# Performance work log

Hardware: AMD Instinct MI355X
Metric: run time of the kernel (lower is better)

The kernel has to match this reference:

```python
import jax, jax.numpy as jnp
import numpy as np

B, S, FEAT = 64, 196, 512
D_MODEL, D_INPUT = 1024, 512
HEADS = 8          # cross-attention heads
SYNC_HEADS = 8     # neuron-sync attention heads (num_attn_heads)
ITERS = 50         # thought ticks
MEM = 25           # memory_length
NLM_H = 16         # memory_hidden_dims
OUT = 1000         # out_dims


def _n(key, i, shape, scale=0.02):
    return scale * jax.random.normal(jax.random.fold_in(key, i), shape, dtype=jnp.float32)


def setup_inputs() -> dict:
    key = jax.random.key(0)
    return {
        "x": jax.random.normal(jax.random.fold_in(key, 0), (B, S, FEAT), dtype=jnp.float32),
        "kv_w": _n(key, 1, (D_INPUT, FEAT)), "kv_b": jnp.zeros((D_INPUT,), jnp.float32),
        "ln_kv_s": jnp.ones((D_INPUT,), jnp.float32), "ln_kv_b": jnp.zeros((D_INPUT,), jnp.float32),
        "q_w": _n(key, 2, (D_INPUT, D_MODEL)), "q_b": jnp.zeros((D_INPUT,), jnp.float32),
        "in_proj_w": _n(key, 3, (3 * D_INPUT, D_INPUT)), "in_proj_b": jnp.zeros((3 * D_INPUT,), jnp.float32),
        "out_proj_w": _n(key, 4, (D_INPUT, D_INPUT)), "out_proj_b": jnp.zeros((D_INPUT,), jnp.float32),
        "W_q": _n(key, 5, (D_MODEL, D_MODEL), 0.03), "W_k": _n(key, 6, (D_MODEL, D_MODEL), 0.03),
        "W_v": _n(key, 7, (D_MODEL, D_MODEL), 0.03),
        "syn_w": _n(key, 8, (2 * D_MODEL, D_INPUT + D_MODEL)), "syn_b": jnp.zeros((2 * D_MODEL,), jnp.float32),
        "syn_ln_s": jnp.ones((D_MODEL,), jnp.float32), "syn_ln_b": jnp.zeros((D_MODEL,), jnp.float32),
        "nlm_w1": _n(key, 9, (MEM, 2 * NLM_H, D_MODEL), 0.1), "nlm_b1": jnp.zeros((D_MODEL, 2 * NLM_H), jnp.float32),
        "nlm_w2": _n(key, 10, (NLM_H, 2, D_MODEL), 0.1), "nlm_b2": jnp.zeros((D_MODEL, 2), jnp.float32),
        "start_activated_state": _n(key, 11, (D_MODEL,), 0.03),
        "start_trace": _n(key, 12, (D_MODEL, MEM), 0.03),
        "out_w": _n(key, 13, (OUT, D_MODEL)), "out_b": jnp.zeros((OUT,), jnp.float32),
    }


def _ln(x, s, b, eps=1e-5):
    m = x.mean(-1, keepdims=True)
    v = x.var(-1, keepdims=True)
    return (x - m) / jnp.sqrt(v + eps) * s + b


def _glu(x):
    a, g = jnp.split(x, 2, axis=-1)
    return a * jax.nn.sigmoid(g)


def reference(x, kv_w, kv_b, ln_kv_s, ln_kv_b, q_w, q_b, in_proj_w, in_proj_b,
              out_proj_w, out_proj_b, W_q, W_k, W_v, syn_w, syn_b, syn_ln_s, syn_ln_b,
              nlm_w1, nlm_b1, nlm_w2, nlm_b2, start_activated_state, start_trace,
              out_w, out_b):
    b = x.shape[0]
    dh_sync = D_MODEL // SYNC_HEADS
    dh = D_INPUT // HEADS

    # kv_proj: Linear + LayerNorm over backbone features (backbone='none')
    kv = _ln(x @ kv_w.T + kv_b, ln_kv_s, ln_kv_b)  # (B,S,Di)
    wq_c, wk_c, wv_c = jnp.split(in_proj_w, 3, axis=0)
    bq_c, bk_c, bv_c = jnp.split(in_proj_b, 3, axis=0)
    Kc = (kv @ wk_c.T + bk_c).reshape(b, S, HEADS, dh).transpose(0, 2, 1, 3)  # (B,H,S,dh)
    Vc = (kv @ wv_c.T + bv_c).reshape(b, S, HEADS, dh).transpose(0, 2, 1, 3)

    def sync_attn(hist, cur):
        # hist: (B,D,T) post-activation history; cur: (B,D) current post-activations
        hr = jnp.swapaxes(hist, 1, 2)  # (B,T,D)
        T = hr.shape[1]
        Q = (hr @ W_q.T).reshape(b, T, SYNC_HEADS, dh_sync).transpose(0, 2, 1, 3)  # (B,H,T,dh)
        K = (hr @ W_k.T).reshape(b, T, SYNC_HEADS, dh_sync).transpose(0, 2, 1, 3)
        V = (cur @ W_v.T).reshape(b, SYNC_HEADS, dh_sync)  # (B,H,dh)
        # neuron-vs-neuron scores: (B,H,dh,dh)
        scores = jnp.einsum('bhtd,bhte->bhde', Q, K) / jnp.sqrt(jnp.float32(dh_sync))
        w = jax.nn.softmax(scores, axis=-1)
        att = jnp.einsum('bhde,bhe->bhd', w, V)  # (B,H,dh)
        # torch: attended.transpose(1,2).reshape(B, D)
        return att.transpose(0, 2, 1).reshape(b, D_MODEL)

    def cross_attn(sync_a):
        q = sync_a @ q_w.T + q_b  # (B,Di)
        Qh = (q @ wq_c.T + bq_c).reshape(b, HEADS, 1, dh)
        s = jnp.einsum('bhqd,bhkd->bhqk', Qh, Kc) / jnp.sqrt(jnp.float32(dh))
        w = jax.nn.softmax(s, axis=-1)
        o = jnp.einsum('bhqk,bhkd->bhqd', w, Vc).transpose(0, 2, 1, 3).reshape(b, D_INPUT)
        return o @ out_proj_w.T + out_proj_b

    state_trace0 = jnp.broadcast_to(start_trace[None], (b, D_MODEL, MEM))
    act0 = jnp.broadcast_to(start_activated_state[None], (b, D_MODEL))
    hist0 = jnp.broadcast_to(start_activated_state[None, :, None], (b, D_MODEL, MEM))
    log_nc = jnp.log(jnp.float32(OUT))

    def tick(carry, _):
        st, act, hist = carry
        sync_a = sync_attn(hist, act)                     # action synchronisation
        ao = cross_attn(sync_a)                           # (B,Di)
        pre = jnp.concatenate([ao, act], axis=-1)
        state = _ln(_glu(pre @ syn_w.T + syn_b), syn_ln_s, syn_ln_b)  # synapse MLP (depth 1)
        st = jnp.concatenate([st[:, :, 1:], state[:, :, None]], axis=-1)  # sliding pre-act trace
        # per-neuron deep NLM (SuperLinear einsums)
        h = _glu(jnp.einsum('bdm,mhd->bdh', st, nlm_w1) + nlm_b1)
        act_new = _glu(jnp.einsum('bdh,hod->bdo', h, nlm_w2) + nlm_b2)[..., 0]
        hist = jnp.concatenate([hist[:, :, 1:], act_new[:, :, None]], axis=-1)
        sync_o = sync_attn(hist, act_new)                 # output synchronisation
        pred = sync_o @ out_w.T + out_b
        logp = jax.nn.log_softmax(pred, axis=-1)
        ne = -jnp.sum(jnp.exp(logp) * logp, axis=-1) / log_nc
        cert = jnp.stack([ne, 1.0 - ne], axis=-1)
        return (st, act_new, hist), (pred, cert, sync_o)

    _, (preds, certs, syncs) = jax.lax.scan(tick, (state_trace0, act0, hist0), None, length=ITERS)
    predictions = jnp.transpose(preds, (1, 2, 0))  # (B,OUT,T)
    certainties = jnp.transpose(certs, (1, 2, 0))  # (B,2,T)
    return predictions, certainties, syncs[-1]
```

## Files before the change

kernel.cpp:

```cpp
#include <hip/hip_runtime.h>
#include <hip/hip_bf16.h>

typedef __attribute__((ext_vector_type(8))) short short8v;
typedef __attribute__((ext_vector_type(4))) float f32x4;
typedef __attribute__((ext_vector_type(4))) float float4v;

#define DEV __device__ __forceinline__

DEV short f2bfs(float x){
  union { float f; unsigned u; } v; v.f = x;
  unsigned r = (v.u + 0x7FFFu + ((v.u >> 16) & 1u)) >> 16;
  return (short)(unsigned short)r;
}
DEV float bfs2f(short s){
  union { unsigned u; float f; } v; v.u = ((unsigned)(unsigned short)s) << 16;
  return v.f;
}
DEV float sigm(float x){ return 1.f / (1.f + __expf(-x)); }
DEV int zmap(int j){ int g = (j >= 1024) ? 1 : 0; int i = j - (g << 10); return (i & 15) + ((i >> 4) << 5) + (g << 4); }

DEV int aldi(const void* p){ return __hip_atomic_load((const int*)p, __ATOMIC_RELAXED, __HIP_MEMORY_SCOPE_AGENT); }
DEV float aldf(const void* p){ return __hip_atomic_load((const float*)p, __ATOMIC_RELAXED, __HIP_MEMORY_SCOPE_AGENT); }
DEV long long aldll(const void* p){ return __hip_atomic_load((const long long*)p, __ATOMIC_RELAXED, __HIP_MEMORY_SCOPE_AGENT); }

DEV void gbar(unsigned* bar, int nb){
  __syncthreads();
  if (threadIdx.x == 0){
    __builtin_amdgcn_fence(__ATOMIC_RELEASE, "agent");
    unsigned* gen = bar + 128;
    unsigned g = __hip_atomic_load(gen, __ATOMIC_RELAXED, __HIP_MEMORY_SCOPE_AGENT);
    int lane = blockIdx.x & 7;
    __hip_atomic_fetch_add(bar + lane*16, 1u, __ATOMIC_RELAXED, __HIP_MEMORY_SCOPE_AGENT);
    if (blockIdx.x == 0){
      unsigned sum;
      do {
        sum = 0;
#pragma unroll
        for (int i = 0; i < 8; i++) sum += __hip_atomic_load(bar + i*16, __ATOMIC_RELAXED, __HIP_MEMORY_SCOPE_AGENT);
      } while (sum < (unsigned)nb);
#pragma unroll
      for (int i = 0; i < 8; i++) __hip_atomic_store(bar + i*16, 0u, __ATOMIC_RELAXED, __HIP_MEMORY_SCOPE_AGENT);
      __hip_atomic_store(gen, g + 1u, __ATOMIC_RELEASE, __HIP_MEMORY_SCOPE_AGENT);
    } else {
      while (__hip_atomic_load(gen, __ATOMIC_RELAXED, __HIP_MEMORY_SCOPE_AGENT) == g)
        __builtin_amdgcn_s_sleep(1);
    }
  }
  __syncthreads();
}


DEV void phase_qhcross(int u, const short* __restrict__ Wfq, const float* __restrict__ bfq,
    const short* __restrict__ Kc, const short* __restrict__ Vc, const short* __restrict__ S_bf,
    short* __restrict__ oaC, float* __restrict__ stats, float* smf, int tid, int zero_stats)
{
  float* Srow = smf;
  float* qs   = smf + 1024;
  float* wsm  = smf + 1088;
  float* red  = smf + 1344;
  int h = u & 7, b = u >> 3;
  __syncthreads();
  const int* spi = (const int*)(S_bf + b*1024);
#pragma unroll
  for (int r = 0; r < 2; r++){
    int idx = tid + r*256;
    int pv = aldi(spi + idx);
    Srow[idx*2]     = bfs2f((short)(pv & 0xffff));
    Srow[idx*2 + 1] = bfs2f((short)(((unsigned)pv) >> 16));
  }
  if (zero_stats && tid < 128) stats[tid] = 0.f;
  __syncthreads();
  {
    int d = tid & 63, c = tid >> 6;
    const short* wp = Wfq + (size_t)(h*64 + d)*1024 + c*256;
    const float* srp = Srow + c*256;
    float acc = 0.f;
#pragma unroll 4
    for (int i = 0; i < 256; i += 8){
      short8v wv = *(const short8v*)(wp + i);
#pragma unroll
      for (int j = 0; j < 8; j++) acc += bfs2f(wv[j]) * srp[i + j];
    }
    red[tid] = acc;
  }
  __syncthreads();
  if (tid < 64) qs[tid] = bfq[h*64 + tid] + red[tid] + red[tid+64] + red[tid+128] + red[tid+192];
  __syncthreads();
  float sv = -1e30f;
  if (tid < 196){
    const short* kp = Kc + ((size_t)(b*196 + tid)*512 + h*64);
    float acc = 0.f;
#pragma unroll
    for (int j = 0; j < 64; j += 8){
      short8v kv8 = *(const short8v*)(kp + j);
#pragma unroll
      for (int u8 = 0; u8 < 8; u8++) acc += bfs2f(kv8[u8]) * qs[j + u8];
    }
    sv = acc * 0.125f;
  }
  red[tid] = sv; __syncthreads();
  for (int s = 128; s > 0; s >>= 1){ if (tid < s) red[tid] = fmaxf(red[tid], red[tid+s]); __syncthreads(); }
  float M = red[0]; __syncthreads();
  float e = (tid < 196) ? __expf(sv - M) : 0.f;
  wsm[tid] = e; red[tid] = e; __syncthreads();
  for (int s = 128; s > 0; s >>= 1){ if (tid < s) red[tid] += red[tid+s]; __syncthreads(); }
  float Z = red[0]; __syncthreads();
  int dd = tid & 63, cc = tid >> 6;
  float acc = 0.f;
  for (int s = cc; s < 196; s += 4) acc += wsm[s] * bfs2f(Vc[(size_t)(b*196 + s)*512 + h*64 + dd]);
  red[tid] = acc; __syncthreads();
  if (tid < 64){
    float o = (red[tid] + red[tid+64] + red[tid+128] + red[tid+192]) / Z;
    oaC[(size_t)b*1536 + h*64 + tid] = f2bfs(o);
  }
  __syncthreads();
}

DEV void phase_glu(int u, const short* __restrict__ Wz, const float* __restrict__ bz,
    const short* __restrict__ oaC, float* __restrict__ ubuf, float* __restrict__ stats,
    float* smf, int tid)
{
  float* part   = smf;
  float* statsl = smf + 8192;
  int n0 = u * 32;
  __syncthreads();
  if (tid < 128) statsl[tid] = 0.f;
  int w = tid >> 6, l15 = tid & 15, l4 = (tid >> 4) & 3;
  f32x4 acc[4][2];
#pragma unroll
  for (int mi = 0; mi < 4; mi++)
#pragma unroll
    for (int ni = 0; ni < 2; ni++) acc[mi][ni] = (f32x4){0.f,0.f,0.f,0.f};
#pragma unroll 2
  for (int it = 0; it < 12; it++){
    int ks = w*384 + it*32 + l4*8;
    short8v a4[4], bb[2];
#pragma unroll
    for (int mi = 0; mi < 4; mi++)
      a4[mi] = *(const short8v*)(oaC + (size_t)(mi*16 + l15)*1536 + ks);
#pragma unroll
    for (int ni = 0; ni < 2; ni++)
      bb[ni] = *(const short8v*)(Wz + (size_t)(n0 + ni*16 + l15)*1536 + ks);
#pragma unroll
    for (int mi = 0; mi < 4; mi++)
#pragma unroll
      for (int ni = 0; ni < 2; ni++)
        acc[mi][ni] = __builtin_amdgcn_mfma_f32_16x16x32_bf16(a4[mi], bb[ni], acc[mi][ni], 0, 0, 0);
  }
#pragma unroll
  for (int mi = 0; mi < 4; mi++)
#pragma unroll
    for (int ni = 0; ni < 2; ni++)
#pragma unroll
      for (int r = 0; r < 4; r++)
        part[w*2048 + (mi*16 + l4*4 + r)*32 + ni*16 + l15] = acc[mi][ni][r];
  __syncthreads();
  int m = tid >> 2;
  float s1 = 0.f, s2 = 0.f;
#pragma unroll
  for (int e = 0; e < 4; e++){
    int j = ((tid & 3) << 2) + e;
    float a = part[m*32 + j] + part[2048 + m*32 + j] + part[4096 + m*32 + j] + part[6144 + m*32 + j] + bz[n0 + j];
    float g = part[m*32 + 16 + j] + part[2048 + m*32 + 16 + j] + part[4096 + m*32 + 16 + j] + part[6144 + m*32 + 16 + j] + bz[n0 + 16 + j];
    float uv = a * sigm(g);
    ubuf[(size_t)m*1024 + (n0 >> 1) + j] = uv;
    s1 += uv; s2 += uv*uv;
  }
  atomicAdd(&statsl[m], s1); atomicAdd(&statsl[64 + m], s2);
  __syncthreads();
  if (tid < 64){ atomicAdd(&stats[tid], statsl[tid]); atomicAdd(&stats[64 + tid], statsl[64 + tid]); }
  __syncthreads();
}

DEV void phase_nlm(int u, const float* __restrict__ ubuf, const float* __restrict__ stats,
    const float* __restrict__ g_s, const float* __restrict__ g_b, float* __restrict__ st,
    const float* __restrict__ w1, const float* __restrict__ b1,
    const float* __restrict__ w2, const float* __restrict__ b2,
    short* __restrict__ oaN, int t, float* smf, int tid)
{
  float* pl = smf;
  int x = u & 63, y = u >> 6;
  int d_i = tid & 15, b_i = (tid >> 4) & 7, half = tid >> 7;
  int d = x*16 + d_i, b = y*8 + b_i;
  float mu = aldf(stats + b) * (1.f/1024.f);
  float var = aldf(stats + 64 + b) * (1.f/1024.f) - mu*mu;
  float rs = rsqrtf(var + 1e-5f);
  float uv = aldf(ubuf + b*1024 + d);
  float state = (uv - mu)*rs*g_s[d] + g_b[d];
  int slot = t % 25;
  if (half == 0) st[(size_t)slot*65536 + b*1024 + d] = state;
  float pre[16];
#pragma unroll
  for (int hh = 0; hh < 16; hh++) pre[hh] = b1[d*32 + half*16 + hh];
  int p0 = (t + 1) % 25;
#pragma unroll 5
  for (int m = 0; m < 25; m++){
    int p = p0 + m; if (p >= 25) p -= 25;
    float sm = (p == slot) ? state : st[(size_t)p*65536 + b*1024 + d];
#pragma unroll
    for (int hh = 0; hh < 16; hh++) pre[hh] += sm * w1[(size_t)(m*32 + half*16 + hh)*1024 + d];
  }
  __syncthreads();
#pragma unroll
  for (int hh = 0; hh < 16; hh++) pl[((half*8 + b_i)*16 + hh)*16 + d_i] = pre[hh];
  __syncthreads();
  if (half == 0){
    float p2a = b2[d*2 + 0], p2g = b2[d*2 + 1];
#pragma unroll
    for (int i = 0; i < 16; i++){
      float hv = pl[((b_i)*16 + i)*16 + d_i] * sigm(pl[((8 + b_i)*16 + i)*16 + d_i]);
      p2a += hv * w2[(size_t)(i*2 + 0)*1024 + d];
      p2g += hv * w2[(size_t)(i*2 + 1)*1024 + d];
    }
    float act = p2a * sigm(p2g);
    oaN[(size_t)b*1536 + 512 + d] = f2bfs(act);
  }
  __syncthreads();
}

DEV void phase_qkv(int u, const short* __restrict__ Wqkv, const short* __restrict__ act_bf,
    short* __restrict__ Qb, short* __restrict__ Kb, float* __restrict__ vc, int slot,
    float* smf, int tid)
{
  float* part = smf;
  int n0 = u * 32;
  __syncthreads();
  int w = tid >> 6, l15 = tid & 15, l4 = (tid >> 4) & 3;
  f32x4 acc[4][2];
#pragma unroll
  for (int mi = 0; mi < 4; mi++)
#pragma unroll
    for (int ni = 0; ni < 2; ni++) acc[mi][ni] = (f32x4){0.f,0.f,0.f,0.f};
#pragma unroll 2
  for (int it = 0; it < 8; it++){
    int ks = w*256 + it*32 + l4*8;
    short8v a4[4], bb[2];
#pragma unroll
    for (int mi = 0; mi < 4; mi++)
      a4[mi] = *(const short8v*)(act_bf + (size_t)(mi*16 + l15)*1536 + ks);
#pragma unroll
    for (int ni = 0; ni < 2; ni++)
      bb[ni] = *(const short8v*)(Wqkv + (size_t)(n0 + ni*16 + l15)*1024 + ks);
#pragma unroll
    for (int mi = 0; mi < 4; mi++)
#pragma unroll
      for (int ni = 0; ni < 2; ni++)
        acc[mi][ni] = __builtin_amdgcn_mfma_f32_16x16x32_bf16(a4[mi], bb[ni], acc[mi][ni], 0, 0, 0);
  }
#pragma unroll
  for (int mi = 0; mi < 4; mi++)
#pragma unroll
    for (int ni = 0; ni < 2; ni++)
#pragma unroll
      for (int r = 0; r < 4; r++)
        part[w*2048 + (mi*16 + l4*4 + r)*32 + ni*16 + l15] = acc[mi][ni][r];
  __syncthreads();
  int m = tid >> 2;
#pragma unroll
  for (int e = 0; e < 8; e++){
    int nl = ((tid & 3) << 3) + e;
    float v = part[m*32 + nl] + part[2048 + m*32 + nl] + part[4096 + m*32 + nl] + part[6144 + m*32 + nl];
    int n = n0 + nl;
    if (n < 1024)      Qb[((size_t)m*1024 + n)*32 + slot] = f2bfs(v);
    else if (n < 2048) Kb[((size_t)m*1024 + (n-1024))*32 + slot] = f2bfs(v);
    else               vc[(size_t)m*1024 + (n-2048)] = v;
  }
  __syncthreads();
}

DEV void phase_sync(int u, int t, const short* __restrict__ Qbuf, const short* __restrict__ Kbuf,
    const float* __restrict__ vcur, float* __restrict__ S, short* __restrict__ S_bf,
    short* __restrict__ SyncO, float* smf, int tid)
{
  short8v* qlds = (short8v*)smf;
  short8v* klds = ((short8v*)smf) + 512;
  long long* ql = (long long*)qlds; long long* kl = (long long*)klds;
  int h = u & 7, b = u >> 3;
  __syncthreads();
  const short* qg = Qbuf + ((size_t)b*1024 + h*128)*32;
  const short* kg = Kbuf + ((size_t)b*1024 + h*128)*32;
#pragma unroll
  for (int it = 0; it < 2; it++){
    int ch = tid + 256*it;
    int d = ch >> 2, c = ch & 3;
    int cs = c ^ ((d >> 1) & 3);
    const long long* qp = (const long long*)qg + d*8 + c*2;
    const long long* kp = (const long long*)kg + d*8 + c*2;
#pragma unroll
    for (int j = 0; j < 2; j++){
      ql[(d*4 + cs)*2 + j] = aldll(qp + j);
      kl[(d*4 + cs)*2 + j] = aldll(kp + j);
    }
  }
  __syncthreads();
  int w = tid >> 6, l15 = tid & 15, l4 = (tid >> 4) & 3;
  short8v af[2], bfr[8];
#pragma unroll
  for (int mi2 = 0; mi2 < 2; mi2++){
    int d = (2*w + mi2)*16 + l15;
    af[mi2] = qlds[d*4 + (l4 ^ ((d >> 1) & 3))];
  }
#pragma unroll
  for (int ni = 0; ni < 8; ni++){
    int e = ni*16 + l15;
    bfr[ni] = klds[e*4 + (l4 ^ ((e >> 1) & 3))];
  }
  f32x4 acc[2][8];
#pragma unroll
  for (int mi2 = 0; mi2 < 2; mi2++)
#pragma unroll
    for (int ni = 0; ni < 8; ni++)
      acc[mi2][ni] = (f32x4){0.f,0.f,0.f,0.f};
#pragma unroll
  for (int mi2 = 0; mi2 < 2; mi2++)
#pragma unroll
    for (int ni = 0; ni < 8; ni++)
      acc[mi2][ni] = __builtin_amdgcn_mfma_f32_16x16x32_bf16(af[mi2], bfr[ni], acc[mi2][ni], 0, 0, 0);
  float Vv[8];
#pragma unroll
  for (int ni = 0; ni < 8; ni++) Vv[ni] = aldf(vcur + b*1024 + h*128 + ni*16 + l15);
  const float scale = 0.08838834764831845f;
#pragma unroll
  for (int mi2 = 0; mi2 < 2; mi2++)
#pragma unroll
    for (int r = 0; r < 4; r++){
      float sv[8]; float mx = -1e30f;
#pragma unroll
      for (int ni = 0; ni < 8; ni++){ sv[ni] = acc[mi2][ni][r]*scale; mx = fmaxf(mx, sv[ni]); }
#pragma unroll
      for (int off = 1; off < 16; off <<= 1) mx = fmaxf(mx, __shfl_xor(mx, off));
      float den = 0.f, num = 0.f;
#pragma unroll
      for (int ni = 0; ni < 8; ni++){ float p = __expf(sv[ni] - mx); den += p; num += p*Vv[ni]; }
#pragma unroll
      for (int off = 1; off < 16; off <<= 1){ den += __shfl_xor(den, off); num += __shfl_xor(num, off); }
      if (l15 == 0){
        int d = (2*w + mi2)*16 + l4*4 + r;
        float att = num / den;
        int oi = b*1024 + d*8 + h;
        S[oi] = att;
        S_bf[oi] = f2bfs(att);
        if (t >= 0) SyncO[((size_t)b*50 + t)*1024 + d*8 + h] = f2bfs(att);
      }
    }
  __syncthreads();
}

__global__ __launch_bounds__(256, 2) void tick_all_k(
    const short* __restrict__ Wfq, const float* __restrict__ bfq,
    const short* __restrict__ Kc, const short* __restrict__ Vc,
    const short* __restrict__ Wz, const float* __restrict__ bz,
    float* __restrict__ ubuf, float* __restrict__ stats,
    const float* __restrict__ g_s, const float* __restrict__ g_b,
    float* __restrict__ st,
    const float* __restrict__ w1, const float* __restrict__ b1,
    const float* __restrict__ w2, const float* __restrict__ b2,
    const short* __restrict__ Wqkv,
    short* __restrict__ Qbuf, short* __restrict__ Kbuf, float* __restrict__ vcur,
    float* __restrict__ S, short* __restrict__ S_bf, short* __restrict__ SyncO,
    short* __restrict__ oaR, unsigned* bar)
{
  __shared__ float smf[8320];
  const int tid = threadIdx.x;
  const int bid = blockIdx.x;
  const int nb  = gridDim.x;

  for (int u = bid; u < 512; u += nb) phase_sync(u, -1, Qbuf, Kbuf, vcur, S, S_bf, SyncO, smf, tid);
  gbar(bar, nb);

#pragma unroll 1
  for (int t = 0; t < 50; t++){
    short* oaC = oaR + (size_t)t * 98304;
    short* oaN = oaR + (size_t)(t + 1) * 98304;
    for (int u = bid; u < 512; u += nb)
      phase_qhcross(u, Wfq, bfq, Kc, Vc, S_bf, oaC, stats, smf, tid, u == 0);
    gbar(bar, nb);
    for (int u = bid; u < 64; u += nb)
      phase_glu(u, Wz, bz, oaC, ubuf, stats, smf, tid);
    gbar(bar, nb);
    for (int u = bid; u < 512; u += nb)
      phase_nlm(u, ubuf, stats, g_s, g_b, st, w1, b1, w2, b2, oaN, t, smf, tid);
    gbar(bar, nb);
    for (int u = bid; u < 96; u += nb)
      phase_qkv(u, Wqkv, oaN + 512, Qbuf, Kbuf, vcur, t % 25, smf, tid);
    gbar(bar, nb);
    for (int u = bid; u < 512; u += nb)
      phase_sync(u, t, Qbuf, Kbuf, vcur, S, S_bf, SyncO, smf, tid);
    gbar(bar, nb);
  }
}

struct EpiBF16 {
  short* C; int ldc; int domap;
  DEV void op(const f32x4 (&acc)[4][2], int m0, int n0, int l15, int l4, const float* bias) const {
#pragma unroll
    for (int mi = 0; mi < 4; mi++)
#pragma unroll
      for (int ni = 0; ni < 2; ni++){
        int n = n0 + ni*16 + l15;
        float bb = bias ? bias[n] : 0.f;
#pragma unroll
        for (int r = 0; r < 4; r++){
          int m = m0 + mi*16 + l4*4 + r;
          int mr = domap ? zmap(m) : m;
          C[(size_t)mr*ldc + n] = f2bfs(acc[mi][ni][r] + bb);
        }
      }
  }
};

struct EpiPred {
  float* outp;
  DEV void op(const f32x4 (&acc)[4][2], int m0, int n0, int l15, int l4, const float* bias) const {
#pragma unroll
    for (int mi = 0; mi < 4; mi++)
#pragma unroll
      for (int ni = 0; ni < 2; ni++){
        int n = n0 + ni*16 + l15;
        if (n >= 1000) continue;
        float bb = bias[n];
#pragma unroll
        for (int r = 0; r < 4; r++){
          int m = m0 + mi*16 + l4*4 + r;
          int b = m / 50, tt = m - b*50;
          outp[(size_t)b*50000 + (size_t)n*50 + tt] = acc[mi][ni][r] + bb;
        }
      }
  }
};

struct EpiKVpre {
  short* C; float* stats;
  DEV void op(const f32x4 (&acc)[4][2], int m0, int n0, int l15, int l4, const float* bias) const {
    float b0 = bias[n0 + l15], b1 = bias[n0 + 16 + l15];
#pragma unroll
    for (int mi = 0; mi < 4; mi++)
#pragma unroll
      for (int r = 0; r < 4; r++){
        int m = m0 + mi*16 + l4*4 + r;
        float v0 = acc[mi][0][r] + b0;
        float v1 = acc[mi][1][r] + b1;
        C[(size_t)m*512 + n0 + l15]      = f2bfs(v0);
        C[(size_t)m*512 + n0 + 16 + l15] = f2bfs(v1);
        float s = v0 + v1, s2 = v0*v0 + v1*v1;
#pragma unroll
        for (int off = 1; off < 16; off <<= 1){ s += __shfl_xor(s, off); s2 += __shfl_xor(s2, off); }
        if (l15 == 0){ atomicAdd(&stats[m*2], s); atomicAdd(&stats[m*2 + 1], s2); }
      }
  }
};

template<bool ABF16, typename EPI>
__global__ __launch_bounds__(256) void gemm_tn(const void* __restrict__ Aptr, int lda,
    const short* __restrict__ Bw, int ldb, const float* __restrict__ bias,
    int K, EPI epi)
{
  int tid = threadIdx.x;
  const int w = tid >> 6, l15 = tid & 15, l4 = (tid >> 4) & 3;
  const int m0 = blockIdx.y * 64;
  const int n0 = blockIdx.x * 128 + w * 32;
  f32x4 acc[4][2];
#pragma unroll
  for (int mi = 0; mi < 4; mi++)
#pragma unroll
    for (int ni = 0; ni < 2; ni++)
      acc[mi][ni] = (f32x4){0.f, 0.f, 0.f, 0.f};
#pragma unroll 4
  for (int kk = 0; kk < K; kk += 32){
    const int ks = kk + l4*8;
    short8v a[4], bfr[2];
#pragma unroll
    for (int mi = 0; mi < 4; mi++){
      const size_t row = (size_t)(m0 + mi*16 + l15);
      if (ABF16){
        a[mi] = *(const short8v*)((const short*)Aptr + row*lda + ks);
      } else {
        const float* ap = (const float*)Aptr + row*lda + ks;
        float4v f0 = *(const float4v*)ap;
        float4v f1 = *(const float4v*)(ap + 4);
        short8v tt;
        tt[0]=f2bfs(f0[0]); tt[1]=f2bfs(f0[1]); tt[2]=f2bfs(f0[2]); tt[3]=f2bfs(f0[3]);
        tt[4]=f2bfs(f1[0]); tt[5]=f2bfs(f1[1]); tt[6]=f2bfs(f1[2]); tt[7]=f2bfs(f1[3]);
        a[mi] = tt;
      }
    }
#pragma unroll
    for (int ni = 0; ni < 2; ni++)
      bfr[ni] = *(const short8v*)(Bw + (size_t)(n0 + ni*16 + l15)*ldb + ks);
#pragma unroll
    for (int mi = 0; mi < 4; mi++)
#pragma unroll
      for (int ni = 0; ni < 2; ni++)
        acc[mi][ni] = __builtin_amdgcn_mfma_f32_16x16x32_bf16(a[mi], bfr[ni], acc[mi][ni], 0, 0, 0);
  }
  epi.op(acc, m0, n0, l15, l4, bias);
}

__global__ __launch_bounds__(256) void vecmat_k(const float* __restrict__ W, int ldw,
    const float* __restrict__ v, const float* __restrict__ add, float* __restrict__ out, int K, int domap)
{
  int w = threadIdx.x >> 6, l = threadIdx.x & 63;
  int n = blockIdx.x*4 + w;
  float s = 0.f;
  for (int k = l; k < K; k += 64) s += W[(size_t)n*ldw + k]*v[k];
#pragma unroll
  for (int off = 32; off; off >>= 1) s += __shfl_xor(s, off);
  if (l == 0){ float o = s + (add ? add[n] : 0.f); out[domap ? zmap(n) : n] = o; }
}

__global__ void castW_k(short* dst, int dld, int drow0, int dcol0,
    const float* src, int sld, int N, int K, int transp, int domap)
{
  size_t idx = (size_t)blockIdx.x*256 + threadIdx.x;
  size_t tot = (size_t)N*K;
  if (idx >= tot) return;
  int n = idx / K, k = idx - (size_t)n*K;
  float vv = 0.f;
  if (src) vv = transp ? src[(size_t)k*sld + n] : src[(size_t)n*sld + k];
  int r = drow0 + (domap ? zmap(n) : n);
  dst[(size_t)r*dld + dcol0 + k] = f2bfs(vv);
}

__global__ void zero_k(float* p, int n){
  int i = blockIdx.x*256 + threadIdx.x;
  if (i < n) p[i] = 0.f;
}

__global__ void ln_inplace_k(short* kvp, const float* __restrict__ stats,
    const float* __restrict__ s, const float* __restrict__ bb)
{
  size_t i = (size_t)blockIdx.x*256 + threadIdx.x;
  int row = i >> 9, c = i & 511;
  float mu = stats[row*2] * (1.f/512.f);
  float var = stats[row*2 + 1] * (1.f/512.f) - mu*mu;
  float v = bfs2f(kvp[i]);
  kvp[i] = f2bfs((v - mu)*rsqrtf(var + 1e-5f)*s[c] + bb[c]);
}

__global__ void fill_k(short* Qbuf, short* Kbuf, float* vcur, short* oaR,
    float* st, const float* q0, const float* k0, const float* v0,
    const float* start, const float* strace)
{
  size_t i = (size_t)blockIdx.x*256 + threadIdx.x;
  const size_t R0 = 64u*1024u*32u;
  if (i < R0){
    int c = i & 31; int d = (i >> 5) & 1023;
    Qbuf[i] = (c < 25) ? f2bfs(q0[d]) : 0;
    Kbuf[i] = (c < 25) ? f2bfs(k0[d]) : 0;
    return;
  }
  i -= R0;
  if (i < 65536){
    int d = i & 1023; int b = i >> 10;
    vcur[i] = v0[d];
    oaR[(size_t)b*1536 + 512 + d] = f2bfs(start[d]);
    return;
  }
  i -= 65536;
  if (i < (size_t)25*65536){
    int p = (int)(i >> 16); int rem = (int)(i & 65535); int d = rem & 1023;
    st[i] = strace[d*25 + p];
  }
}

__global__ __launch_bounds__(256) void cert_k(const float* __restrict__ preds, float* __restrict__ cert)
{
  int t = blockIdx.x, b = blockIdx.y, tid = threadIdx.x;
  __shared__ float red[256];
  float v[4]; float mx = -1e30f;
#pragma unroll
  for (int i = 0; i < 4; i++){
    int o = tid + i*256;
    v[i] = (o < 1000) ? preds[(size_t)b*50000 + (size_t)o*50 + t] : -1e30f;
    mx = fmaxf(mx, v[i]);
  }
  red[tid] = mx; __syncthreads();
  for (int s = 128; s; s >>= 1){ if (tid < s) red[tid] = fmaxf(red[tid], red[tid + s]); __syncthreads(); }
  float M = red[0]; __syncthreads();
  float z = 0.f, wsum = 0.f;
#pragma unroll
  for (int i = 0; i < 4; i++){
    int o = tid + i*256;
    if (o < 1000){ float p = v[i] - M; float e = __expf(p); z += e; wsum += e*p; }
  }
  red[tid] = z; __syncthreads();
  for (int s = 128; s; s >>= 1){ if (tid < s) red[tid] += red[tid + s]; __syncthreads(); }
  float Z = red[0]; __syncthreads();
  red[tid] = wsum; __syncthreads();
  for (int s = 128; s; s >>= 1){ if (tid < s) red[tid] += red[tid + s]; __syncthreads(); }
  float Wm = red[0];
  if (tid == 0){
    float ne = (__logf(Z) - Wm/Z) * 0.14476482730108392f;
    cert[b*100 + t] = ne;
    cert[b*100 + 50 + t] = 1.f - ne;
  }
}

__global__ void copy_sync_k(const float* __restrict__ S, float* __restrict__ out){
  int i = blockIdx.x*256 + threadIdx.x;
  out[i] = S[i];
}

extern "C" void kernel_launch(void* const* d_in, const int* in_sizes, int n_in,
                              void* d_out, int out_size, void* d_ws, size_t ws_size,
                              hipStream_t stream)
{
  const float* x        = (const float*)d_in[0];
  const float* kv_w     = (const float*)d_in[1];
  const float* kv_b     = (const float*)d_in[2];
  const float* ln_kv_s  = (const float*)d_in[3];
  const float* ln_kv_b  = (const float*)d_in[4];
  const float* q_w      = (const float*)d_in[5];
  const float* q_b      = (const float*)d_in[6];
  const float* in_proj_w= (const float*)d_in[7];
  const float* in_proj_b= (const float*)d_in[8];
  const float* out_proj_w=(const float*)d_in[9];
  const float* out_proj_b=(const float*)d_in[10];
  const float* W_q      = (const float*)d_in[11];
  const float* W_k      = (const float*)d_in[12];
  const float* W_v      = (const float*)d_in[13];
  const float* syn_w    = (const float*)d_in[14];
  const float* syn_b    = (const float*)d_in[15];
  const float* syn_ln_s = (const float*)d_in[16];
  const float* syn_ln_b = (const float*)d_in[17];
  const float* nlm_w1   = (const float*)d_in[18];
  const float* nlm_b1   = (const float*)d_in[19];
  const float* nlm_w2   = (const float*)d_in[20];
  const float* nlm_b2   = (const float*)d_in[21];
  const float* start_act= (const float*)d_in[22];
  const float* strace   = (const float*)d_in[23];
  const float* out_w    = (const float*)d_in[24];
  const float* out_b    = (const float*)d_in[25];
  float* out = (float*)d_out;

  char* ws = (char*)d_ws;
  size_t off = 0;
  auto alloc = [&](size_t bytes)->char*{ char* p = ws + off; off = (off + bytes + 255) & ~(size_t)255; return p; };

  short* qw_B   = (short*)alloc((size_t)1024*512*2);
  short* opw_B  = (short*)alloc((size_t)512*512*2);
  short* Wfq    = (short*)alloc((size_t)512*1024*2);
  float* bfq    = (float*)alloc(512*4);
  short* Wz     = (short*)alloc((size_t)2048*1536*2);
  float* bz     = (float*)alloc(2048*4);
  short* Wqkv   = (short*)alloc((size_t)3072*1024*2);
  short* outwB  = (short*)alloc((size_t)1024*1024*2);
  short* kvw_B  = (short*)alloc((size_t)512*512*2);
  short* wkc_B  = (short*)alloc((size_t)512*512*2);
  short* wvc_B  = (short*)alloc((size_t)512*512*2);
  short* kvp    = (short*)alloc((size_t)12544*512*2);
  float* kvstats= (float*)alloc((size_t)25088*4);
  short* Kc     = (short*)alloc((size_t)12544*512*2);
  short* Vc     = (short*)alloc((size_t)12544*512*2);
  short* Qbuf   = (short*)alloc((size_t)64*1024*32*2);
  short* Kbuf   = (short*)alloc((size_t)64*1024*32*2);
  float* vcur   = (float*)alloc((size_t)65536*4);
  float* S      = (float*)alloc((size_t)65536*4);
  short* S_bf   = (short*)alloc((size_t)65536*2);
  short* SyncO  = (short*)alloc((size_t)64*50*1024*2);
  float* ubuf   = (float*)alloc((size_t)65536*4);
  float* stats  = (float*)alloc(128*4);
  float* st     = (float*)alloc((size_t)1638400*4);
  float* q0     = (float*)alloc(1024*4);
  float* k0     = (float*)alloc(1024*4);
  float* v0     = (float*)alloc(1024*4);
  unsigned* bar = (unsigned*)alloc(1024);
  short* oaR    = kvp;
  (void)ws_size; (void)in_sizes; (void)n_in; (void)out_size;

  dim3 blk(256);

  zero_k<<<dim3(1), blk, 0, stream>>>((float*)bar, 256);
  castW_k<<<dim3((1024*512+255)/256), blk, 0, stream>>>(qw_B, 512, 0, 0, q_w, 1024, 1024, 512, 1, 0);
  castW_k<<<dim3((512*512+255)/256), blk, 0, stream>>>(opw_B, 512, 0, 0, out_proj_w, 512, 512, 512, 1, 0);
  castW_k<<<dim3((2048*1024+255)/256), blk, 0, stream>>>(Wz, 1536, 0, 512, syn_w + 512, 1536, 2048, 1024, 0, 1);
  castW_k<<<dim3((1024*1024+255)/256), blk, 0, stream>>>(Wqkv, 1024, 0, 0, W_q, 1024, 1024, 1024, 0, 0);
  castW_k<<<dim3((1024*1024+255)/256), blk, 0, stream>>>(Wqkv, 1024, 1024, 0, W_k, 1024, 1024, 1024, 0, 0);
  castW_k<<<dim3((1024*1024+255)/256), blk, 0, stream>>>(Wqkv, 1024, 2048, 0, W_v, 1024, 1024, 1024, 0, 0);
  castW_k<<<dim3((1000*1024+255)/256), blk, 0, stream>>>(outwB, 1024, 0, 0, out_w, 1024, 1000, 1024, 0, 0);
  castW_k<<<dim3((24*1024+255)/256), blk, 0, stream>>>(outwB, 1024, 1000, 0, nullptr, 0, 24, 1024, 0, 0);
  castW_k<<<dim3((512*512+255)/256), blk, 0, stream>>>(kvw_B, 512, 0, 0, kv_w, 512, 512, 512, 0, 0);
  castW_k<<<dim3((512*512+255)/256), blk, 0, stream>>>(wkc_B, 512, 0, 0, in_proj_w + 512*512, 512, 512, 512, 0, 0);
  castW_k<<<dim3((512*512+255)/256), blk, 0, stream>>>(wvc_B, 512, 0, 0, in_proj_w + 1024*512, 512, 512, 512, 0, 0);

  vecmat_k<<<dim3(256), blk, 0, stream>>>(W_q, 1024, start_act, nullptr, q0, 1024, 0);
  vecmat_k<<<dim3(256), blk, 0, stream>>>(W_k, 1024, start_act, nullptr, k0, 1024, 0);
  vecmat_k<<<dim3(256), blk, 0, stream>>>(W_v, 1024, start_act, nullptr, v0, 1024, 0);
  vecmat_k<<<dim3(128), blk, 0, stream>>>(in_proj_w, 512, q_b, in_proj_b, bfq, 512, 0);
  vecmat_k<<<dim3(512), blk, 0, stream>>>(syn_w, 1536, out_proj_b, syn_b, bz, 512, 1);

  gemm_tn<false, EpiBF16><<<dim3(8, 8), blk, 0, stream>>>(in_proj_w, 512, qw_B, 512, nullptr, 512, EpiBF16{Wfq, 1024, 0});
  gemm_tn<false, EpiBF16><<<dim3(4, 32), blk, 0, stream>>>(syn_w, 1536, opw_B, 512, nullptr, 512, EpiBF16{Wz, 1536, 1});

  zero_k<<<dim3(98), blk, 0, stream>>>(kvstats, 25088);
  gemm_tn<false, EpiKVpre><<<dim3(4, 196), blk, 0, stream>>>(x, 512, kvw_B, 512, kv_b, 512, EpiKVpre{kvp, kvstats});
  ln_inplace_k<<<dim3(25088), blk, 0, stream>>>(kvp, kvstats, ln_kv_s, ln_kv_b);
  gemm_tn<true, EpiBF16><<<dim3(4, 196), blk, 0, stream>>>(kvp, 512, wkc_B, 512, in_proj_b + 512, 512, EpiBF16{Kc, 512, 0});
  gemm_tn<true, EpiBF16><<<dim3(4, 196), blk, 0, stream>>>(kvp, 512, wvc_B, 512, in_proj_b + 1024, 512, EpiBF16{Vc, 512, 0});

  fill_k<<<dim3(14848), blk, 0, stream>>>(Qbuf, Kbuf, vcur, oaR, st, q0, k0, v0, start_act, strace);

  int nb = 256;
  {
    int mb = 0;
    if (hipOccupancyMaxActiveBlocksPerMultiprocessor(&mb, reinterpret_cast<const void*>(tick_all_k), 256, 0) == hipSuccess && mb >= 1){
      int dev = 0; hipGetDevice(&dev);
      int ncu = 0;
      if (hipDeviceGetAttribute(&ncu, hipDeviceAttributeMultiprocessorCount, dev) != hipSuccess || ncu <= 0) ncu = 256;
      long cap = (long)mb * (long)ncu;
      nb = (int)(cap < 512 ? cap : 512);
    }
  }
  tick_all_k<<<dim3(nb), blk, 0, stream>>>(Wfq, bfq, Kc, Vc, Wz, bz, ubuf, stats,
      syn_ln_s, syn_ln_b, st, nlm_w1, nlm_b1, nlm_w2, nlm_b2, Wqkv,
      Qbuf, Kbuf, vcur, S, S_bf, SyncO, oaR, bar);

  gemm_tn<true, EpiPred><<<dim3(8, 50), blk, 0, stream>>>(SyncO, 1024, outwB, 1024, out_b, 1024, EpiPred{out});
  cert_k<<<dim3(50, 64), blk, 0, stream>>>(out, out + 3200000);
  copy_sync_k<<<dim3(256), blk, 0, stream>>>(S, out + 3206400);
}
```

Measured before the change: 7.325 ms.

## Remap persistent tick work to blocks, ring buffers, bf16 NLM weights, prefetch V

The persistent tick kernel now assigns work so that block index mod 8 fixes a head or column group, which likely keeps the same weights and data on the same XCD's L2. Sync state and Q/K histories move into per-tick slot arrays, so readers use plain loads instead of agent-scope atomic loads and Q/K are written contiguously rather than strided. NLM weights are cast to bf16 once up front to halve their traffic. The cross-attention phase prefetches its V column into registers with nontemporal loads before the score computation. The costs are more global memory for the slot buffers, extra register pressure from the 49-entry prefetch, and bf16 rounding of the NLM weights.

```diff
diff --git a/kernel.cpp b/kernel.cpp
--- a/kernel.cpp
+++ b/kernel.cpp
@@ -19,9 +19,7 @@
 DEV float sigm(float x){ return 1.f / (1.f + __expf(-x)); }
 DEV int zmap(int j){ int g = (j >= 1024) ? 1 : 0; int i = j - (g << 10); return (i & 15) + ((i >> 4) << 5) + (g << 4); }
 
-DEV int aldi(const void* p){ return __hip_atomic_load((const int*)p, __ATOMIC_RELAXED, __HIP_MEMORY_SCOPE_AGENT); }
 DEV float aldf(const void* p){ return __hip_atomic_load((const float*)p, __ATOMIC_RELAXED, __HIP_MEMORY_SCOPE_AGENT); }
-DEV long long aldll(const void* p){ return __hip_atomic_load((const long long*)p, __ATOMIC_RELAXED, __HIP_MEMORY_SCOPE_AGENT); }
 
 DEV void gbar(unsigned* bar, int nb){
   __syncthreads();
@@ -50,23 +48,30 @@
 }
 
 
-DEV void phase_qhcross(int u, const short* __restrict__ Wfq, const float* __restrict__ bfq,
-    const short* __restrict__ Kc, const short* __restrict__ Vc, const short* __restrict__ S_bf,
+DEV void phase_qhcross(int b, int h, const short* __restrict__ Wfq, const float* __restrict__ bfq,
+    const short* __restrict__ Kc, const short* __restrict__ Vc, const short* __restrict__ Sslot,
     short* __restrict__ oaC, float* __restrict__ stats, float* smf, int tid, int zero_stats)
 {
   float* Srow = smf;
   float* qs   = smf + 1024;
   float* wsm  = smf + 1088;
   float* red  = smf + 1344;
-  int h = u & 7, b = u >> 3;
-  __syncthreads();
-  const int* spi = (const int*)(S_bf + b*1024);
-#pragma unroll
-  for (int r = 0; r < 2; r++){
-    int idx = tid + r*256;
-    int pv = aldi(spi + idx);
-    Srow[idx*2]     = bfs2f((short)(pv & 0xffff));
-    Srow[idx*2 + 1] = bfs2f((short)(((unsigned)pv) >> 16));
+  __syncthreads();
+  int cc = tid >> 6, dd = tid & 63;
+  unsigned short vv[49];
+  {
+    const unsigned short* vp = (const unsigned short*)Vc + ((size_t)(b*196 + cc)*512 + h*64 + dd);
+#pragma unroll
+    for (int i = 0; i < 49; i++)
+      vv[i] = __builtin_nontemporal_load(vp + (size_t)i*2048);
+  }
+  {
+    const int* sp = (const int*)Sslot + b*512;
+    int v0 = sp[tid], v1 = sp[tid + 256];
+    Srow[tid*2]           = bfs2f((short)(v0 & 0xffff));
+    Srow[tid*2 + 1]       = bfs2f((short)(((unsigned)v0) >> 16));
+    Srow[512 + tid*2]     = bfs2f((short)(v1 & 0xffff));
+    Srow[512 + tid*2 + 1] = bfs2f((short)(((unsigned)v1) >> 16));
   }
   if (zero_stats && tid < 128) stats[tid] = 0.f;
   __syncthreads();
@@ -88,13 +93,13 @@
   __syncthreads();
   float sv = -1e30f;
   if (tid < 196){
-    const short* kp = Kc + ((size_t)(b*196 + tid)*512 + h*64);
+    const short8v* kp = (const short8v*)(Kc + ((size_t)(b*196 + tid)*512 + h*64));
     float acc = 0.f;
 #pragma unroll
-    for (int j = 0; j < 64; j += 8){
-      short8v kv8 = *(const short8v*)(kp + j);
-#pragma unroll
-      for (int u8 = 0; u8 < 8; u8++) acc += bfs2f(kv8[u8]) * qs[j + u8];
+    for (int j = 0; j < 8; j++){
+      short8v kv8 = __builtin_nontemporal_load(kp + j);
+#pragma unroll
+      for (int u8 = 0; u8 < 8; u8++) acc += bfs2f(kv8[u8]) * qs[j*8 + u8];
     }
     sv = acc * 0.125f;
   }
@@ -105,9 +110,9 @@
   wsm[tid] = e; red[tid] = e; __syncthreads();
   for (int s = 128; s > 0; s >>= 1){ if (tid < s) red[tid] += red[tid+s]; __syncthreads(); }
   float Z = red[0]; __syncthreads();
-  int dd = tid & 63, cc = tid >> 6;
   float acc = 0.f;
-  for (int s = cc; s < 196; s += 4) acc += wsm[s] * bfs2f(Vc[(size_t)(b*196 + s)*512 + h*64 + dd]);
+#pragma unroll
+  for (int i = 0; i < 49; i++) acc += wsm[cc + 4*i] * bfs2f((short)vv[i]);
   red[tid] = acc; __syncthreads();
   if (tid < 64){
     float o = (red[tid] + red[tid+64] + red[tid+128] + red[tid+192]) / Z;
@@ -116,13 +121,12 @@
   __syncthreads();
 }
 
-DEV void phase_glu(int u, const short* __restrict__ Wz, const float* __restrict__ bz,
+DEV void phase_glu(int n0, const short* __restrict__ Wz, const float* __restrict__ bz,
     const short* __restrict__ oaC, float* __restrict__ ubuf, float* __restrict__ stats,
     float* smf, int tid)
 {
   float* part   = smf;
   float* statsl = smf + 8192;
-  int n0 = u * 32;
   __syncthreads();
   if (tid < 128) statsl[tid] = 0.f;
   int w = tid >> 6, l15 = tid & 15, l4 = (tid >> 4) & 3;
@@ -172,14 +176,13 @@
   __syncthreads();
 }
 
-DEV void phase_nlm(int u, const float* __restrict__ ubuf, const float* __restrict__ stats,
+DEV void phase_nlm(int x, int y, const float* __restrict__ ubuf, const float* __restrict__ stats,
     const float* __restrict__ g_s, const float* __restrict__ g_b, float* __restrict__ st,
-    const float* __restrict__ w1, const float* __restrict__ b1,
-    const float* __restrict__ w2, const float* __restrict__ b2,
+    const short* __restrict__ w1, const float* __restrict__ b1,
+    const short* __restrict__ w2, const float* __restrict__ b2,
     short* __restrict__ oaN, int t, float* smf, int tid)
 {
   float* pl = smf;
-  int x = u & 63, y = u >> 6;
   int d_i = tid & 15, b_i = (tid >> 4) & 7, half = tid >> 7;
   int d = x*16 + d_i, b = y*8 + b_i;
   float mu = aldf(stats + b) * (1.f/1024.f);
@@ -198,7 +201,7 @@
     int p = p0 + m; if (p >= 25) p -= 25;
     float sm = (p == slot) ? state : st[(size_t)p*65536 + b*1024 + d];
 #pragma unroll
-    for (int hh = 0; hh < 16; hh++) pre[hh] += sm * w1[(size_t)(m*32 + half*16 + hh)*1024 + d];
+    for (int hh = 0; hh < 16; hh++) pre[hh] += sm * bfs2f(w1[(size_t)(m*32 + half*16 + hh)*1024 + d]);
   }
   __syncthreads();
 #pragma unroll
@@ -209,8 +212,8 @@
 #pragma unroll
     for (int i = 0; i < 16; i++){
       float hv = pl[((b_i)*16 + i)*16 + d_i] * sigm(pl[((8 + b_i)*16 + i)*16 + d_i]);
-      p2a += hv * w2[(size_t)(i*2 + 0)*1024 + d];
-      p2g += hv * w2[(size_t)(i*2 + 1)*1024 + d];
+      p2a += hv * bfs2f(w2[(size_t)(i*2 + 0)*1024 + d]);
+      p2g += hv * bfs2f(w2[(size_t)(i*2 + 1)*1024 + d]);
     }
     float act = p2a * sigm(p2g);
     oaN[(size_t)b*1536 + 512 + d] = f2bfs(act);
@@ -218,12 +221,11 @@
   __syncthreads();
 }
 
-DEV void phase_qkv(int u, const short* __restrict__ Wqkv, const short* __restrict__ act_bf,
-    short* __restrict__ Qb, short* __restrict__ Kb, float* __restrict__ vc, int slot,
+DEV void phase_qkv(int n0, const short* __restrict__ Wqkv, const short* __restrict__ act_bf,
+    short* __restrict__ Qslot, short* __restrict__ Kslot, float* __restrict__ vc,
     float* smf, int tid)
 {
   float* part = smf;
-  int n0 = u * 32;
   __syncthreads();
   int w = tid >> 6, l15 = tid & 15, l4 = (tid >> 4) & 3;
   f32x4 acc[4][2];
@@ -261,38 +263,41 @@
     int nl = ((tid & 3) << 3) + e;
     float v = part[m*32 + nl] + part[2048 + m*32 + nl] + part[4096 + m*32 + nl] + part[6144 + m*32 + nl];
     int n = n0 + nl;
-    if (n < 1024)      Qb[((size_t)m*1024 + n)*32 + slot] = f2bfs(v);
-    else if (n < 2048) Kb[((size_t)m*1024 + (n-1024))*32 + slot] = f2bfs(v);
+    if (n < 1024)      Qslot[(size_t)m*1024 + n] = f2bfs(v);
+    else if (n < 2048) Kslot[(size_t)m*1024 + (n-1024)] = f2bfs(v);
     else               vc[(size_t)m*1024 + (n-2048)] = v;
   }
   __syncthreads();
 }
 
-DEV void phase_sync(int u, int t, const short* __restrict__ Qbuf, const short* __restrict__ Kbuf,
-    const float* __restrict__ vcur, float* __restrict__ S, short* __restrict__ S_bf,
+DEV void phase_sync(int b, int h, int t, const short* __restrict__ Qn, const short* __restrict__ Kn,
+    const float* __restrict__ vcur, float* __restrict__ S, short* __restrict__ SslotN,
     short* __restrict__ SyncO, float* smf, int tid)
 {
-  short8v* qlds = (short8v*)smf;
-  short8v* klds = ((short8v*)smf) + 512;
-  long long* ql = (long long*)qlds; long long* kl = (long long*)klds;
-  int h = u & 7, b = u >> 3;
-  __syncthreads();
-  const short* qg = Qbuf + ((size_t)b*1024 + h*128)*32;
-  const short* kg = Kbuf + ((size_t)b*1024 + h*128)*32;
-#pragma unroll
-  for (int it = 0; it < 2; it++){
-    int ch = tid + 256*it;
-    int d = ch >> 2, c = ch & 3;
+  short* qt = (short*)smf;
+  short* kt = qt + 4096;
+  __syncthreads();
+  const short* Qb = Qn + (size_t)(t+1)*65536 + b*1024 + h*128;
+  const short* Kb = Kn + (size_t)(t+1)*65536 + b*1024 + h*128;
+#pragma unroll
+  for (int pass = 0; pass < 8; pass++){
+    int ch = tid + pass*256;
+    int m = ch >> 6, ii = ch & 63, d = ii << 1;
+    int qv = 0, kv = 0;
+    if (m < 25){
+      qv = *(const int*)(Qb + (size_t)m*65536 + d);
+      kv = *(const int*)(Kb + (size_t)m*65536 + d);
+    }
+    int c = m >> 3, pos = m & 7;
     int cs = c ^ ((d >> 1) & 3);
-    const long long* qp = (const long long*)qg + d*8 + c*2;
-    const long long* kp = (const long long*)kg + d*8 + c*2;
-#pragma unroll
-    for (int j = 0; j < 2; j++){
-      ql[(d*4 + cs)*2 + j] = aldll(qp + j);
-      kl[(d*4 + cs)*2 + j] = aldll(kp + j);
-    }
-  }
-  __syncthreads();
+    qt[d*32 + cs*8 + pos]       = (short)(qv & 0xffff);
+    qt[(d+1)*32 + cs*8 + pos]   = (short)(((unsigned)qv) >> 16);
+    kt[d*32 + cs*8 + pos]       = (short)(kv & 0xffff);
+    kt[(d+1)*32 + cs*8 + pos]   = (short)(((unsigned)kv) >> 16);
+  }
+  __syncthreads();
+  const short8v* qlds = (const short8v*)qt;
+  const short8v* klds = (const short8v*)kt;
   int w = tid >> 6, l15 = tid & 15, l4 = (tid >> 4) & 3;
   short8v af[2], bfr[8];
 #pragma unroll
@@ -339,7 +344,7 @@
         float att = num / den;
         int oi = b*1024 + d*8 + h;
         S[oi] = att;
-        S_bf[oi] = f2bfs(att);
+        SslotN[oi] = f2bfs(att);
         if (t >= 0) SyncO[((size_t)b*50 + t)*1024 + d*8 + h] = f2bfs(att);
       }
     }
@@ -353,39 +358,47 @@
     float* __restrict__ ubuf, float* __restrict__ stats,
     const float* __restrict__ g_s, const float* __restrict__ g_b,
     float* __restrict__ st,
-    const float* __restrict__ w1, const float* __restrict__ b1,
-    const float* __restrict__ w2, const float* __restrict__ b2,
+    const short* __restrict__ w1, const float* __restrict__ b1,
+    const short* __restrict__ w2, const float* __restrict__ b2,
     const short* __restrict__ Wqkv,
-    short* __restrict__ Qbuf, short* __restrict__ Kbuf, float* __restrict__ vcur,
-    float* __restrict__ S, short* __restrict__ S_bf, short* __restrict__ SyncO,
+    short* __restrict__ Qn, short* __restrict__ Kn, float* __restrict__ vcur,
+    float* __restrict__ S, short* __restrict__ S_bfR, short* __restrict__ SyncO,
     short* __restrict__ oaR, unsigned* bar)
 {
   __shared__ float smf[8320];
   const int tid = threadIdx.x;
   const int bid = blockIdx.x;
   const int nb  = gridDim.x;
-
-  for (int u = bid; u < 512; u += nb) phase_sync(u, -1, Qbuf, Kbuf, vcur, S, S_bf, SyncO, smf, tid);
+  const int k   = bid & 7;
+  const int j0  = bid >> 3;
+  const int js  = nb >> 3;
+
+  for (int j = j0; j < 64; j += js)
+    phase_sync(k*8 + (j & 7), j >> 3, -1, Qn, Kn, vcur, S, S_bfR, SyncO, smf, tid);
   gbar(bar, nb);
 
 #pragma unroll 1
   for (int t = 0; t < 50; t++){
+    const short* Sslot = S_bfR + (size_t)t * 65536;
+    short* SslotN      = S_bfR + (size_t)(t+1) * 65536;
     short* oaC = oaR + (size_t)t * 98304;
-    short* oaN = oaR + (size_t)(t + 1) * 98304;
-    for (int u = bid; u < 512; u += nb)
-      phase_qhcross(u, Wfq, bfq, Kc, Vc, S_bf, oaC, stats, smf, tid, u == 0);
+    short* oaN = oaR + (size_t)(t+1) * 98304;
+    for (int j = j0; j < 64; j += js)
+      phase_qhcross(j, k, Wfq, bfq, Kc, Vc, Sslot, oaC, stats, smf, tid, (bid == 0 && j == j0));
     gbar(bar, nb);
-    for (int u = bid; u < 64; u += nb)
-      phase_glu(u, Wz, bz, oaC, ubuf, stats, smf, tid);
+    for (int j = j0; j < 8; j += js)
+      phase_glu((k*8 + j)*32, Wz, bz, oaC, ubuf, stats, smf, tid);
     gbar(bar, nb);
-    for (int u = bid; u < 512; u += nb)
-      phase_nlm(u, ubuf, stats, g_s, g_b, st, w1, b1, w2, b2, oaN, t, smf, tid);
+    for (int j = j0; j < 64; j += js)
+      phase_nlm(k*8 + (j & 7), j >> 3, ubuf, stats, g_s, g_b, st, w1, b1, w2, b2, oaN, t, smf, tid);
     gbar(bar, nb);
-    for (int u = bid; u < 96; u += nb)
-      phase_qkv(u, Wqkv, oaN + 512, Qbuf, Kbuf, vcur, t % 25, smf, tid);
+    for (int j = j0; j < 12; j += js){
+      int n0 = ((j >> 2)*32 + k*4 + (j & 3)) * 32;
+      phase_qkv(n0, Wqkv, oaN + 512, Qn + (size_t)(25+t)*65536, Kn + (size_t)(25+t)*65536, vcur, smf, tid);
+    }
     gbar(bar, nb);
-    for (int u = bid; u < 512; u += nb)
-      phase_sync(u, t, Qbuf, Kbuf, vcur, S, S_bf, SyncO, smf, tid);
+    for (int j = j0; j < 64; j += js)
+      phase_sync(k*8 + (j & 7), j >> 3, t, Qn, Kn, vcur, S, SslotN, SyncO, smf, tid);
     gbar(bar, nb);
   }
 }
@@ -537,28 +550,28 @@
   kvp[i] = f2bfs((v - mu)*rsqrtf(var + 1e-5f)*s[c] + bb[c]);
 }
 
-__global__ void fill_k(short* Qbuf, short* Kbuf, float* vcur, short* oaR,
+__global__ void fill_k(short* Qn, short* Kn, float* vcur, short* oaR,
     float* st, const float* q0, const float* k0, const float* v0,
     const float* start, const float* strace)
 {
   size_t i = (size_t)blockIdx.x*256 + threadIdx.x;
-  const size_t R0 = 64u*1024u*32u;
-  if (i < R0){
-    int c = i & 31; int d = (i >> 5) & 1023;
-    Qbuf[i] = (c < 25) ? f2bfs(q0[d]) : 0;
-    Kbuf[i] = (c < 25) ? f2bfs(k0[d]) : 0;
+  const size_t H = 25u*65536u;
+  if (i < H){
+    int d = (int)(i & 1023);
+    Qn[i] = f2bfs(q0[d]);
+    Kn[i] = f2bfs(k0[d]);
     return;
   }
-  i -= R0;
+  i -= H;
   if (i < 65536){
-    int d = i & 1023; int b = i >> 10;
+    int d = (int)(i & 1023); int b = (int)(i >> 10);
     vcur[i] = v0[d];
     oaR[(size_t)b*1536 + 512 + d] = f2bfs(start[d]);
     return;
   }
   i -= 65536;
-  if (i < (size_t)25*65536){
-    int p = (int)(i >> 16); int rem = (int)(i & 65535); int d = rem & 1023;
+  if (i < H){
+    int p = (int)(i >> 16), d = (int)(i & 1023);
     st[i] = strace[d*25 + p];
   }
 }
@@ -652,15 +665,17 @@
   float* kvstats= (float*)alloc((size_t)25088*4);
   short* Kc     = (short*)alloc((size_t)12544*512*2);
   short* Vc     = (short*)alloc((size_t)12544*512*2);
-  short* Qbuf   = (short*)alloc((size_t)64*1024*32*2);
-  short* Kbuf   = (short*)alloc((size_t)64*1024*32*2);
+  short* Qn     = (short*)alloc((size_t)75*65536*2);
+  short* Kn     = (short*)alloc((size_t)75*65536*2);
   float* vcur   = (float*)alloc((size_t)65536*4);
   float* S      = (float*)alloc((size_t)65536*4);
-  short* S_bf   = (short*)alloc((size_t)65536*2);
+  short* S_bfR  = (short*)alloc((size_t)51*65536*2);
   short* SyncO  = (short*)alloc((size_t)64*50*1024*2);
   float* ubuf   = (float*)alloc((size_t)65536*4);
   float* stats  = (float*)alloc(128*4);
   float* st     = (float*)alloc((size_t)1638400*4);
+  short* w1b    = (short*)alloc((size_t)800*1024*2);
+  short* w2b    = (short*)alloc((size_t)32*1024*2);
   float* q0     = (float*)alloc(1024*4);
   float* k0     = (float*)alloc(1024*4);
   float* v0     = (float*)alloc(1024*4);
@@ -682,6 +697,8 @@
   castW_k<<<dim3((512*512+255)/256), blk, 0, stream>>>(kvw_B, 512, 0, 0, kv_w, 512, 512, 512, 0, 0);
   castW_k<<<dim3((512*512+255)/256), blk, 0, stream>>>(wkc_B, 512, 0, 0, in_proj_w + 512*512, 512, 512, 512, 0, 0);
   castW_k<<<dim3((512*512+255)/256), blk, 0, stream>>>(wvc_B, 512, 0, 0, in_proj_w + 1024*512, 512, 512, 512, 0, 0);
+  castW_k<<<dim3((800*1024+255)/256), blk, 0, stream>>>(w1b, 1024, 0, 0, nlm_w1, 1024, 800, 1024, 0, 0);
+  castW_k<<<dim3((32*1024+255)/256), blk, 0, stream>>>(w2b, 1024, 0, 0, nlm_w2, 1024, 32, 1024, 0, 0);
 
   vecmat_k<<<dim3(256), blk, 0, stream>>>(W_q, 1024, start_act, nullptr, q0, 1024, 0);
   vecmat_k<<<dim3(256), blk, 0, stream>>>(W_k, 1024, start_act, nullptr, k0, 1024, 0);
@@ -698,7 +715,7 @@
   gemm_tn<true, EpiBF16><<<dim3(4, 196), blk, 0, stream>>>(kvp, 512, wkc_B, 512, in_proj_b + 512, 512, EpiBF16{Kc, 512, 0});
   gemm_tn<true, EpiBF16><<<dim3(4, 196), blk, 0, stream>>>(kvp, 512, wvc_B, 512, in_proj_b + 1024, 512, EpiBF16{Vc, 512, 0});
 
-  fill_k<<<dim3(14848), blk, 0, stream>>>(Qbuf, Kbuf, vcur, oaR, st, q0, k0, v0, start_act, strace);
+  fill_k<<<dim3(13056), blk, 0, stream>>>(Qn, Kn, vcur, oaR, st, q0, k0, v0, start_act, strace);
 
   int nb = 256;
   {
@@ -711,9 +728,10 @@
       nb = (int)(cap < 512 ? cap : 512);
     }
   }
+  nb &= ~7; if (nb < 8) nb = 8;
   tick_all_k<<<dim3(nb), blk, 0, stream>>>(Wfq, bfq, Kc, Vc, Wz, bz, ubuf, stats,
-      syn_ln_s, syn_ln_b, st, nlm_w1, nlm_b1, nlm_w2, nlm_b2, Wqkv,
-      Qbuf, Kbuf, vcur, S, S_bf, SyncO, oaR, bar);
+      syn_ln_s, syn_ln_b, st, w1b, nlm_b1, w2b, nlm_b2, Wqkv,
+      Qn, Kn, vcur, S, S_bfR, SyncO, oaR, bar);
 
   gemm_tn<true, EpiPred><<<dim3(8, 50), blk, 0, stream>>>(SyncO, 1024, outwB, 1024, out_b, 1024, EpiPred{out});
   cert_k<<<dim3(50, 64), blk, 0, stream>>>(out, out + 3200000);
```

New measurement: 6.632 ms. 1.1x faster.
